# Kernel optimization log

Measured on AMD Instinct MI355X. Metric: run time of the kernel, lower is better.

## Reference

```python
import math
import jax, jax.numpy as jnp
import numpy as np

B, N, TOKEN_DIM = 8, 8192, 512
NODE_DIM = 64
MAX_NODES = 64
SCORE_HIDDEN = 64


def setup_inputs() -> dict:
    key = jax.random.key(0)
    ks = jax.random.split(key, 8)
    s = lambda k, shape, fan_in: jax.random.normal(k, shape, jnp.float32) / np.sqrt(fan_in)
    return {
        "token_feats": jax.random.normal(ks[0], (B, N, TOKEN_DIM), jnp.float32),
        "score_w1": s(ks[1], (TOKEN_DIM, SCORE_HIDDEN), TOKEN_DIM),
        "score_b1": jnp.zeros((SCORE_HIDDEN,), jnp.float32),
        "score_w2": s(ks[2], (SCORE_HIDDEN, 1), SCORE_HIDDEN),
        "score_b2": jnp.zeros((1,), jnp.float32),
        "t2n_w": s(ks[3], (TOKEN_DIM, NODE_DIM), TOKEN_DIM),
        "n2t_w": s(ks[4], (NODE_DIM, TOKEN_DIM), NODE_DIM),
        "gcn_w1": s(ks[5], (NODE_DIM, NODE_DIM), NODE_DIM),
        "gcn_w2": s(ks[6], (NODE_DIM, NODE_DIM), NODE_DIM),
    }


def reference(token_feats, score_w1, score_b1, score_w2, score_b2,
              t2n_w, n2t_w, gcn_w1, gcn_w2):
    Bn, Nn, d = token_feats.shape
    M = MAX_NODES
    eps = 1e-6

    # --- node selection (scores -> threshold -> top-k among selected) ---
    h = jax.nn.relu(jnp.einsum('bnd,dh->bnh', token_feats, score_w1) + score_b1)
    scores = (jnp.einsum('bnh,ho->bno', h, score_w2) + score_b2)[..., 0]  # [B,N]
    mean = scores.mean(axis=1, keepdims=True)
    std = scores.std(axis=1, keepdims=True)  # unbiased=False (population)
    thr = mean + 0.5 * std
    count = jnp.sum(scores > thr, axis=1)  # [B]
    fallback_k = min(M, max(4, Nn // 16))
    take_k = jnp.where(count == 0, fallback_k, jnp.minimum(count, M))  # [B]

    _, top_idx = jax.lax.top_k(scores, M)  # [B,M] highest scores; set == torch's selection
    node_mask = jnp.arange(M)[None, :] < take_k[:, None]  # [B,M] bool
    maskf = node_mask.astype(token_feats.dtype)

    gathered = jnp.take_along_axis(token_feats, top_idx[..., None], axis=1)  # [B,M,d]
    H0 = jnp.einsum('bmd,dk->bmk', gathered, t2n_w) * maskf[..., None]  # [B,M,node_dim]

    # --- cosine-similarity adjacency, masked, self-loops, row-normalized ---
    nrm = jnp.maximum(jnp.linalg.norm(H0, axis=-1, keepdims=True), eps)
    Hn = H0 / nrm
    A = jax.nn.relu(jnp.einsum('bik,bjk->bij', Hn, Hn))
    A = A * (maskf[:, :, None] * maskf[:, None, :])
    A = A + jnp.eye(M, dtype=A.dtype)[None] * maskf[:, None, :]
    A = A / jnp.maximum(A.sum(axis=-1, keepdims=True), 1e-6)

    # --- two-layer GCN (no bias) ---
    x = jax.nn.relu(jnp.einsum('bij,bjk,kl->bil', A, H0, gcn_w1))
    Hg = jax.nn.relu(jnp.einsum('bij,bjk,kl->bil', A, x, gcn_w2))  # [B,M,node_dim]

    # --- attention scatter-back to tokens ---
    token_proj = jnp.einsum('bnd,dk->bnk', token_feats, t2n_w)  # [B,N,node_dim]
    logits = jnp.einsum('bnk,bmk->bnm', token_proj, Hg) / math.sqrt(NODE_DIM)
    attn = jax.nn.softmax(logits, axis=-1)
    injected = jnp.einsum('bnm,bmk->bnk', attn, Hg)
    back = jnp.einsum('bnk,kd->bnd', injected, n2t_w)
    return token_feats + back
```

## Files before the change

kernel.cpp:

```cpp
#include <hip/hip_runtime.h>
#include <hip/hip_bf16.h>

#define B_ 8
#define N_ 8192
#define D_ 512
#define M_ 64

typedef unsigned short u16;
typedef unsigned int u32;
typedef __attribute__((ext_vector_type(8))) short bf16x8;
typedef __attribute__((ext_vector_type(4))) float f32x4;

__device__ __forceinline__ u16 f2bf(float f) {
  u32 u = __float_as_uint(f);
  u += 0x7FFFu + ((u >> 16) & 1u);
  return (u16)(u >> 16);
}
__device__ __forceinline__ float bf2f(u16 h) {
  return __uint_as_float(((u32)h) << 16);
}

__device__ __forceinline__ int bfrag_idx(int kd, int c, int ncols16) {
  int sub = (kd >> 5) * ncols16 + (c >> 4);
  int lane = (c & 15) + 16 * ((kd & 15) >> 2);
  int e = (kd & 3) + 4 * ((kd >> 4) & 1);
  return sub * 512 + lane * 8 + e;
}

__device__ __forceinline__ int kslot(int ln, int e) {
  return (e & 3) + 4 * (ln >> 4) + 16 * (e >> 2);
}

__device__ __forceinline__ bf16x8 pack8(float4 v0, float4 v1) {
  bf16x8 a;
  a[0] = (short)f2bf(v0.x); a[1] = (short)f2bf(v0.y);
  a[2] = (short)f2bf(v0.z); a[3] = (short)f2bf(v0.w);
  a[4] = (short)f2bf(v1.x); a[5] = (short)f2bf(v1.y);
  a[6] = (short)f2bf(v1.z); a[7] = (short)f2bf(v1.w);
  return a;
}

__global__ __launch_bounds__(256) void k_prep(
    const float* __restrict__ t2n, const float* __restrict__ n2t,
    const float* __restrict__ W1, const float* __restrict__ g1,
    const float* __restrict__ g2,
    u16* __restrict__ t2nf, u16* __restrict__ n2tf,
    u16* __restrict__ W1h, u16* __restrict__ W1l,
    u16* __restrict__ g1f, u16* __restrict__ g2f)
{
  const int gid = blockIdx.x * 256 + threadIdx.x;
  const int stride = gridDim.x * 256;
  for (int s = gid; s < 512 * 64; s += stride) {
    const int k = s >> 6, c = s & 63;
    const int idx = bfrag_idx(k, c, 4);
    t2nf[idx] = f2bf(t2n[s]);
    const float w = W1[s];
    const u16 wh = f2bf(w);
    W1h[idx] = wh;
    W1l[idx] = f2bf(w - bf2f(wh));
  }
  for (int s = gid; s < 64 * 512; s += stride) {
    const int k = s >> 9, c = s & 511;
    n2tf[bfrag_idx(k, c, 32)] = f2bf(n2t[s]);
  }
  for (int s = gid; s < 4096; s += stride) {
    const int k = s >> 6, c = s & 63;
    g1f[bfrag_idx(k, c, 4)] = f2bf(g1[s]);
    g2f[bfrag_idx(k, c, 4)] = f2bf(g2[s]);
  }
}

__global__ __launch_bounds__(256, 3) void k_sp(
    const float* __restrict__ X, const u16* __restrict__ W1h,
    const u16* __restrict__ W1l, const u16* __restrict__ t2nf,
    const float* __restrict__ b1, const float* __restrict__ w2,
    const float* __restrict__ b2, float* __restrict__ scores,
    float* __restrict__ outStash)
{
  __shared__ __align__(16) u16 sAf[4096];
  const int tid = threadIdx.x;
  const int t0 = blockIdx.x * 64;
  const int wv = tid >> 6, ln = tid & 63;
  const int lq = ln >> 4, lr = ln & 15;
  u16* mySf = &sAf[wv * 1024];
  const float* xr = X + (size_t)(t0 + 16 * wv + lr) * D_;

  f32x4 acc[4], accP[4];
  #pragma unroll
  for (int cb = 0; cb < 4; ++cb) {
    acc[cb] = (f32x4){0.f, 0.f, 0.f, 0.f};
    accP[cb] = (f32x4){0.f, 0.f, 0.f, 0.f};
  }

  float4 p0[3], p1[3];
  #pragma unroll
  for (int q = 0; q < 3; ++q) {
    p0[q] = *(const float4*)(xr + 32 * q + 4 * lq);
    p1[q] = *(const float4*)(xr + 32 * q + 16 + 4 * lq);
  }

  #pragma unroll
  for (int kb = 0; kb < 16; ++kb) {
    const int slot = kb % 3;
    const float4 v0 = p0[slot], v1 = p1[slot];
    if (kb + 3 < 16) {
      p0[slot] = *(const float4*)(xr + 32 * (kb + 3) + 4 * lq);
      p1[slot] = *(const float4*)(xr + 32 * (kb + 3) + 16 + 4 * lq);
    }
    const float xs[8] = {v0.x, v0.y, v0.z, v0.w, v1.x, v1.y, v1.z, v1.w};
    bf16x8 ah, al;
    #pragma unroll
    for (int e = 0; e < 8; ++e) {
      const u16 h = f2bf(xs[e]);
      ah[e] = (short)h;
      al[e] = (short)f2bf(xs[e] - bf2f(h));
    }
    #pragma unroll
    for (int cb = 0; cb < 4; ++cb) {
      const bf16x8 bh = *(const bf16x8*)&W1h[(kb * 4 + cb) * 512 + ln * 8];
      const bf16x8 bl = *(const bf16x8*)&W1l[(kb * 4 + cb) * 512 + ln * 8];
      const bf16x8 bt = *(const bf16x8*)&t2nf[(kb * 4 + cb) * 512 + ln * 8];
      acc[cb]  = __builtin_amdgcn_mfma_f32_16x16x32_bf16(ah, bh, acc[cb], 0, 0, 0);
      acc[cb]  = __builtin_amdgcn_mfma_f32_16x16x32_bf16(ah, bl, acc[cb], 0, 0, 0);
      acc[cb]  = __builtin_amdgcn_mfma_f32_16x16x32_bf16(al, bh, acc[cb], 0, 0, 0);
      accP[cb] = __builtin_amdgcn_mfma_f32_16x16x32_bf16(ah, bt, accP[cb], 0, 0, 0);
    }
  }

  float b1v[4], w2v[4];
  #pragma unroll
  for (int cb = 0; cb < 4; ++cb) {
    const int col = cb * 16 + lr;
    b1v[cb] = b1[col]; w2v[cb] = w2[col];
  }
  const float b2v = b2[0];
  #pragma unroll
  for (int r = 0; r < 4; ++r) {
    float p = 0.f;
    #pragma unroll
    for (int cb = 0; cb < 4; ++cb) {
      const float h = fmaxf(acc[cb][r] + b1v[cb], 0.f);
      p = fmaf(h, w2v[cb], p);
    }
    p += __shfl_xor(p, 1); p += __shfl_xor(p, 2);
    p += __shfl_xor(p, 4); p += __shfl_xor(p, 8);
    if (lr == 0) scores[t0 + wv * 16 + 4 * lq + r] = p + b2v;
  }

  #pragma unroll
  for (int cb = 0; cb < 4; ++cb)
    #pragma unroll
    for (int r = 0; r < 4; ++r) {
      const int idx = (cb >> 1) * 512 + (4 * lq + r + 16 * (lr >> 2)) * 8 +
                      (lr & 3) + 4 * (cb & 1);
      mySf[idx] = f2bf(accP[cb][r]);
    }
  u16* stash = (u16*)(outStash + (size_t)blockIdx.x * 32768);
  #pragma unroll
  for (int kb2 = 0; kb2 < 2; ++kb2)
    *(bf16x8*)&stash[wv * 1024 + kb2 * 512 + ln * 8] =
        *(const bf16x8*)&mySf[kb2 * 512 + ln * 8];
}

__global__ __launch_bounds__(1024) void k_select(
    const float* __restrict__ scores, int* __restrict__ top_idx,
    int* __restrict__ take_k)
{
  __shared__ float sS[N_];
  __shared__ u32 hist[256];
  __shared__ float redf[34];
  __shared__ u32 redu[16];
  __shared__ u32 sPrefix, sRank, sCntA, sCntT;
  __shared__ int candIdx[64];
  __shared__ float candVal[64];
  __shared__ int tieIdx[128];
  const int b = blockIdx.x, tid = threadIdx.x;
  const int wv = tid >> 6, ln = tid & 63;
  const float* s = scores + (size_t)b * N_;

  float sum = 0.f, sq = 0.f;
  for (int i = tid; i < N_; i += 1024) {
    const float v = s[i]; sS[i] = v; sum += v; sq = fmaf(v, v, sq);
  }
  #pragma unroll
  for (int off = 32; off > 0; off >>= 1) {
    sum += __shfl_xor(sum, off);
    sq  += __shfl_xor(sq, off);
  }
  if (ln == 0) { redf[wv] = sum; redf[16 + wv] = sq; }
  __syncthreads();
  if (tid == 0) {
    float tot = 0.f, totq = 0.f;
    #pragma unroll
    for (int w = 0; w < 16; ++w) { tot += redf[w]; totq += redf[16 + w]; }
    const float mean = tot / (float)N_;
    const float var  = totq / (float)N_ - mean * mean;
    redf[32] = mean + 0.5f * sqrtf(fmaxf(var, 0.f));
  }
  __syncthreads();
  const float thr = redf[32];
  int c = 0;
  for (int i = tid; i < N_; i += 1024) c += (sS[i] > thr) ? 1 : 0;
  #pragma unroll
  for (int off = 32; off > 0; off >>= 1) c += __shfl_xor(c, off);
  if (ln == 0) redu[wv] = (u32)c;
  __syncthreads();
  if (tid == 0) {
    int cnt = 0;
    #pragma unroll
    for (int w = 0; w < 16; ++w) cnt += (int)redu[w];
    take_k[b] = (cnt == 0) ? M_ : (cnt < M_ ? cnt : M_);
  }
  __syncthreads();

  u32 prefix = 0, rank = 64, pmask = 0;
  for (int pass = 0; pass < 4; ++pass) {
    const int shift = 24 - 8 * pass;
    if (tid < 256) hist[tid] = 0;
    __syncthreads();
    for (int i = tid; i < N_; i += 1024) {
      const u32 u = __float_as_uint(sS[i]);
      const u32 key = u ^ ((u32)((int)u >> 31) | 0x80000000u);
      const bool active = (key & pmask) == prefix;
      const int bin = (int)((key >> shift) & 255u);
      if (pass == 0) {
        unsigned long long act = __ballot(active);
        while (act) {
          const int leader = (int)__builtin_ctzll(act);
          const int lbin = __shfl(bin, leader);
          const unsigned long long eq = __ballot(active && (bin == lbin));
          if (ln == leader) atomicAdd(&hist[lbin], (u32)__builtin_popcountll(eq));
          act &= ~eq;
        }
      } else {
        if (active) atomicAdd(&hist[bin], 1u);
      }
    }
    __syncthreads();
    if (tid < 64) {
      const u32 h0 = hist[4 * tid], h1 = hist[4 * tid + 1];
      const u32 h2 = hist[4 * tid + 2], h3 = hist[4 * tid + 3];
      const u32 s3 = h3, s2 = h2 + s3, s1 = h1 + s2, s0 = h0 + s1;
      u32 run = s0;
      #pragma unroll
      for (int off = 1; off < 64; off <<= 1) {
        const u32 t = (u32)__shfl_down((int)run, off);
        if (tid + off < 64) run += t;
      }
      const u32 excl = run - s0;
      const u32 c0 = s0 + excl, c1 = s1 + excl, c2 = s2 + excl, c3 = s3 + excl;
      int pick = -1; u32 nxt = 0;
      if (c0 >= rank && c1 < rank)        { pick = 0; nxt = c1; }
      else if (c1 >= rank && c2 < rank)   { pick = 1; nxt = c2; }
      else if (c2 >= rank && c3 < rank)   { pick = 2; nxt = c3; }
      else if (c3 >= rank && excl < rank) { pick = 3; nxt = excl; }
      if (pick >= 0) {
        sPrefix = prefix | ((u32)(4 * tid + pick) << shift);
        sRank = rank - nxt;
      }
    }
    __syncthreads();
    prefix = sPrefix; rank = sRank;
    pmask |= 0xFFu << shift;
    __syncthreads();
  }

  if (tid == 0) { sCntA = 0; sCntT = 0; }
  __syncthreads();
  const u32 pivot = prefix;
  for (int i = tid; i < N_; i += 1024) {
    const u32 u = __float_as_uint(sS[i]);
    const u32 key = u ^ ((u32)((int)u >> 31) | 0x80000000u);
    if (key > pivot) {
      const u32 p = atomicAdd(&sCntA, 1u);
      candIdx[p] = i; candVal[p] = sS[i];
    } else if (key == pivot) {
      const u32 p = atomicAdd(&sCntT, 1u);
      if (p < 128) tieIdx[p] = i;
    }
  }
  __syncthreads();
  if (tid == 0) {
    const int nA = (int)sCntA;
    const int need = 64 - nA;
    int nT = (int)sCntT; if (nT > 128) nT = 128;
    for (int j = 0; j < need; ++j) {
      int bi = 1 << 30, bp = -1;
      for (int q = 0; q < nT; ++q) {
        const int v = tieIdx[q];
        if (v >= 0 && v < bi) { bi = v; bp = q; }
      }
      candIdx[nA + j] = bi; candVal[nA + j] = sS[bi]; tieIdx[bp] = -1;
    }
  }
  __syncthreads();
  if (tid < 64) {
    const float v = candVal[tid]; const int ii = candIdx[tid];
    int rk = 0;
    for (int j = 0; j < 64; ++j) {
      const float vj = candVal[j]; const int ij = candIdx[j];
      rk += (vj > v || (vj == v && ij < ii)) ? 1 : 0;
    }
    top_idx[b * M_ + rk] = ii;
  }
}

__device__ __forceinline__ bf16x8 ldsA_frag(const float (*S)[65], int wv, int kb, int ln) {
  const int lr = ln & 15;
  bf16x8 a;
  #pragma unroll
  for (int e = 0; e < 8; ++e) a[e] = (short)f2bf(S[16 * wv + lr][32 * kb + kslot(ln, e)]);
  return a;
}
__device__ __forceinline__ bf16x8 ldsB_frag(const float (*S)[65], int cb, int kb, int ln) {
  const int lr = ln & 15;
  bf16x8 bb;
  #pragma unroll
  for (int e = 0; e < 8; ++e) bb[e] = (short)f2bf(S[32 * kb + kslot(ln, e)][16 * cb + lr]);
  return bb;
}
__device__ __forceinline__ bf16x8 ldsBT_frag(const float (*S)[65], int cb, int kb, int ln) {
  const int lr = ln & 15;
  bf16x8 bb;
  #pragma unroll
  for (int e = 0; e < 8; ++e) bb[e] = (short)f2bf(S[16 * cb + lr][32 * kb + kslot(ln, e)]);
  return bb;
}

__global__ __launch_bounds__(256) void k_graph(
    const float* __restrict__ X, const u16* __restrict__ t2nf,
    const u16* __restrict__ n2tf, const u16* __restrict__ g1f,
    const u16* __restrict__ g2f, const int* __restrict__ top_idx,
    const int* __restrict__ take_k, u16* __restrict__ HgTf,
    u16* __restrict__ Wf)
{
  __shared__ float sH0[64][65];
  __shared__ float sA[64][65];
  __shared__ float sT[64][65];
  __shared__ float sU[64][65];
  __shared__ float sR[64];
  const int b = blockIdx.x, tid = threadIdx.x;
  const int wv = tid >> 6, ln = tid & 63;
  const int lq = ln >> 4, lr = ln & 15;
  const int tk = take_k[b];
  const int rowm = 16 * wv + 4 * lq;

  const int gidx = top_idx[b * M_ + 16 * wv + lr];
  const float* xr = X + ((size_t)b * N_ + gidx) * D_;
  f32x4 d[4];
  #pragma unroll
  for (int cb = 0; cb < 4; ++cb) d[cb] = (f32x4){0.f, 0.f, 0.f, 0.f};
  {
    float4 p0[3], p1[3];
    #pragma unroll
    for (int q = 0; q < 3; ++q) {
      p0[q] = *(const float4*)(xr + 32 * q + 4 * lq);
      p1[q] = *(const float4*)(xr + 32 * q + 16 + 4 * lq);
    }
    #pragma unroll
    for (int kb = 0; kb < 16; ++kb) {
      const int slot = kb % 3;
      const float4 v0 = p0[slot], v1 = p1[slot];
      if (kb + 3 < 16) {
        p0[slot] = *(const float4*)(xr + 32 * (kb + 3) + 4 * lq);
        p1[slot] = *(const float4*)(xr + 32 * (kb + 3) + 16 + 4 * lq);
      }
      const bf16x8 a = pack8(v0, v1);
      #pragma unroll
      for (int cb = 0; cb < 4; ++cb) {
        const bf16x8 bb = *(const bf16x8*)&t2nf[(kb * 4 + cb) * 512 + ln * 8];
        d[cb] = __builtin_amdgcn_mfma_f32_16x16x32_bf16(a, bb, d[cb], 0, 0, 0);
      }
    }
  }
  #pragma unroll
  for (int cb = 0; cb < 4; ++cb)
    #pragma unroll
    for (int r = 0; r < 4; ++r)
      sH0[rowm + r][16 * cb + lr] = (rowm + r < tk) ? d[cb][r] : 0.f;
  __syncthreads();

  if (tid < 64) {
    float s = 0.f;
    #pragma unroll
    for (int k = 0; k < 64; ++k) { const float v = sH0[tid][k]; s = fmaf(v, v, s); }
    sR[tid] = 1.f / fmaxf(sqrtf(s), 1e-6f);
  }
  __syncthreads();
  #pragma unroll
  for (int p = 0; p < 16; ++p) {
    const int o = tid + p * 256;
    const int i = o >> 6, k = o & 63;
    sU[i][k] = sH0[i][k] * sR[i];
  }
  __syncthreads();

  #pragma unroll
  for (int cb = 0; cb < 4; ++cb) d[cb] = (f32x4){0.f, 0.f, 0.f, 0.f};
  #pragma unroll
  for (int kb = 0; kb < 2; ++kb) {
    const bf16x8 a = ldsA_frag(sU, wv, kb, ln);
    #pragma unroll
    for (int cb = 0; cb < 4; ++cb)
      d[cb] = __builtin_amdgcn_mfma_f32_16x16x32_bf16(a, ldsBT_frag(sU, cb, kb, ln), d[cb], 0, 0, 0);
  }
  __syncthreads();
  #pragma unroll
  for (int cb = 0; cb < 4; ++cb)
    #pragma unroll
    for (int r = 0; r < 4; ++r) {
      const int row = rowm + r, col = 16 * cb + lr;
      float s = fmaxf(d[cb][r], 0.f);
      s = (row < tk && col < tk) ? s : 0.f;
      if (row == col && row < tk) s += 1.f;
      sA[row][col] = s;
    }
  __syncthreads();

  if (tid < 64) {
    float rs = 0.f;
    #pragma unroll
    for (int j = 0; j < 64; ++j) rs += sA[tid][j];
    sR[tid] = 1.f / fmaxf(rs, 1e-6f);
  }
  __syncthreads();
  #pragma unroll
  for (int p = 0; p < 16; ++p) {
    const int o = tid + p * 256;
    const int i = o >> 6, j = o & 63;
    sA[i][j] *= sR[i];
  }
  __syncthreads();

  #pragma unroll
  for (int cb = 0; cb < 4; ++cb) d[cb] = (f32x4){0.f, 0.f, 0.f, 0.f};
  #pragma unroll
  for (int kb = 0; kb < 2; ++kb) {
    const bf16x8 a = ldsA_frag(sA, wv, kb, ln);
    #pragma unroll
    for (int cb = 0; cb < 4; ++cb)
      d[cb] = __builtin_amdgcn_mfma_f32_16x16x32_bf16(a, ldsB_frag(sH0, cb, kb, ln), d[cb], 0, 0, 0);
  }
  __syncthreads();
  #pragma unroll
  for (int cb = 0; cb < 4; ++cb)
    #pragma unroll
    for (int r = 0; r < 4; ++r) sT[rowm + r][16 * cb + lr] = d[cb][r];
  __syncthreads();

  #pragma unroll
  for (int cb = 0; cb < 4; ++cb) d[cb] = (f32x4){0.f, 0.f, 0.f, 0.f};
  #pragma unroll
  for (int kb = 0; kb < 2; ++kb) {
    const bf16x8 a = ldsA_frag(sT, wv, kb, ln);
    #pragma unroll
    for (int cb = 0; cb < 4; ++cb) {
      const bf16x8 bb = *(const bf16x8*)&g1f[(kb * 4 + cb) * 512 + ln * 8];
      d[cb] = __builtin_amdgcn_mfma_f32_16x16x32_bf16(a, bb, d[cb], 0, 0, 0);
    }
  }
  __syncthreads();
  #pragma unroll
  for (int cb = 0; cb < 4; ++cb)
    #pragma unroll
    for (int r = 0; r < 4; ++r) sU[rowm + r][16 * cb + lr] = fmaxf(d[cb][r], 0.f);
  __syncthreads();

  #pragma unroll
  for (int cb = 0; cb < 4; ++cb) d[cb] = (f32x4){0.f, 0.f, 0.f, 0.f};
  #pragma unroll
  for (int kb = 0; kb < 2; ++kb) {
    const bf16x8 a = ldsA_frag(sA, wv, kb, ln);
    #pragma unroll
    for (int cb = 0; cb < 4; ++cb)
      d[cb] = __builtin_amdgcn_mfma_f32_16x16x32_bf16(a, ldsB_frag(sU, cb, kb, ln), d[cb], 0, 0, 0);
  }
  __syncthreads();
  #pragma unroll
  for (int cb = 0; cb < 4; ++cb)
    #pragma unroll
    for (int r = 0; r < 4; ++r) sT[rowm + r][16 * cb + lr] = d[cb][r];
  __syncthreads();

  #pragma unroll
  for (int cb = 0; cb < 4; ++cb) d[cb] = (f32x4){0.f, 0.f, 0.f, 0.f};
  #pragma unroll
  for (int kb = 0; kb < 2; ++kb) {
    const bf16x8 a = ldsA_frag(sT, wv, kb, ln);
    #pragma unroll
    for (int cb = 0; cb < 4; ++cb) {
      const bf16x8 bb = *(const bf16x8*)&g2f[(kb * 4 + cb) * 512 + ln * 8];
      d[cb] = __builtin_amdgcn_mfma_f32_16x16x32_bf16(a, bb, d[cb], 0, 0, 0);
    }
  }
  __syncthreads();
  #pragma unroll
  for (int cb = 0; cb < 4; ++cb)
    #pragma unroll
    for (int r = 0; r < 4; ++r) {
      const int node = rowm + r, feat = 16 * cb + lr;
      const float hv = fmaxf(d[cb][r], 0.f);
      HgTf[(size_t)b * 4096 + bfrag_idx(feat, node, 4)] = f2bf(hv);
      sU[node][feat] = hv;
    }
  __syncthreads();

  for (int chk = 0; chk < 4; ++chk) {
    f32x4 aw[8];
    #pragma unroll
    for (int c8 = 0; c8 < 8; ++c8) aw[c8] = (f32x4){0.f, 0.f, 0.f, 0.f};
    #pragma unroll
    for (int kbf = 0; kbf < 2; ++kbf) {
      const bf16x8 a = ldsA_frag(sU, wv, kbf, ln);
      #pragma unroll
      for (int c8 = 0; c8 < 8; ++c8) {
        const bf16x8 bb = *(const bf16x8*)&n2tf[(kbf * 32 + chk * 8 + c8) * 512 + ln * 8];
        aw[c8] = __builtin_amdgcn_mfma_f32_16x16x32_bf16(a, bb, aw[c8], 0, 0, 0);
      }
    }
    #pragma unroll
    for (int c8 = 0; c8 < 8; ++c8)
      #pragma unroll
      for (int r = 0; r < 4; ++r) {
        const int m = 16 * wv + 4 * lq + r;
        const int c = (chk * 8 + c8) * 16 + lr;
        Wf[(size_t)b * 32768 + bfrag_idx(m, c, 32)] = f2bf(aw[c8][r]);
      }
  }
}

__global__ __launch_bounds__(256) void k_attn(
    const float* __restrict__ X, const u16* __restrict__ HgTf,
    const u16* __restrict__ Wf, float* __restrict__ out)
{
  __shared__ __align__(16) u16 sAf[4096];
  __shared__ __align__(16) float sBo[4][16][68];
  const int tid = threadIdx.x;
  const int b = blockIdx.x >> 7;
  const int t0 = (blockIdx.x & 127) << 6;
  const float* Xb = X + (size_t)b * N_ * D_;
  float* Ob = out + (size_t)b * N_ * D_;
  const int wv = tid >> 6, ln = tid & 63;
  const int lq = ln >> 4, lr = ln & 15;
  u16* mySf = &sAf[wv * 1024];
  const u16* stash = (const u16*)(out + (size_t)blockIdx.x * 32768);

  f32x4 accL[4];
  #pragma unroll
  for (int cb = 0; cb < 4; ++cb) accL[cb] = (f32x4){0.f, 0.f, 0.f, 0.f};
  #pragma unroll
  for (int kb = 0; kb < 2; ++kb) {
    const bf16x8 a = *(const bf16x8*)&stash[wv * 1024 + kb * 512 + ln * 8];
    #pragma unroll
    for (int cb = 0; cb < 4; ++cb) {
      const bf16x8 bb = *(const bf16x8*)&HgTf[(size_t)b * 4096 + (kb * 4 + cb) * 512 + ln * 8];
      accL[cb] = __builtin_amdgcn_mfma_f32_16x16x32_bf16(a, bb, accL[cb], 0, 0, 0);
    }
  }
  __syncthreads();

  float attnv[4][4];
  #pragma unroll
  for (int r = 0; r < 4; ++r) {
    const float v0 = accL[0][r], v1 = accL[1][r], v2 = accL[2][r], v3 = accL[3][r];
    float mx = fmaxf(fmaxf(v0, v1), fmaxf(v2, v3));
    mx = fmaxf(mx, __shfl_xor(mx, 1)); mx = fmaxf(mx, __shfl_xor(mx, 2));
    mx = fmaxf(mx, __shfl_xor(mx, 4)); mx = fmaxf(mx, __shfl_xor(mx, 8));
    const float e0 = __expf((v0 - mx) * 0.125f), e1 = __expf((v1 - mx) * 0.125f);
    const float e2 = __expf((v2 - mx) * 0.125f), e3 = __expf((v3 - mx) * 0.125f);
    float sm = (e0 + e1) + (e2 + e3);
    sm += __shfl_xor(sm, 1); sm += __shfl_xor(sm, 2);
    sm += __shfl_xor(sm, 4); sm += __shfl_xor(sm, 8);
    const float inv = 1.f / sm;
    attnv[0][r] = e0 * inv; attnv[1][r] = e1 * inv;
    attnv[2][r] = e2 * inv; attnv[3][r] = e3 * inv;
  }
  #pragma unroll
  for (int cb = 0; cb < 4; ++cb)
    #pragma unroll
    for (int r = 0; r < 4; ++r) {
      const int idx = (cb >> 1) * 512 + (4 * lq + r + 16 * (lr >> 2)) * 8 +
                      (lr & 3) + 4 * (cb & 1);
      mySf[idx] = f2bf(attnv[cb][r]);
    }

  for (int chk = 0; chk < 4; ++chk) {
    float4 xres[8];
    #pragma unroll
    for (int h = 0; h < 2; ++h)
      #pragma unroll
      for (int j = 0; j < 4; ++j)
        xres[h * 4 + j] = *(const float4*)(
            Xb + (size_t)(t0 + 16 * wv + 4 * j + lq) * D_ + chk * 128 + h * 64 + 4 * lr);

    f32x4 accB[8];
    #pragma unroll
    for (int c8 = 0; c8 < 8; ++c8) accB[c8] = (f32x4){0.f, 0.f, 0.f, 0.f};
    #pragma unroll
    for (int kb = 0; kb < 2; ++kb) {
      const bf16x8 a = *(const bf16x8*)&mySf[kb * 512 + ln * 8];
      #pragma unroll
      for (int c8 = 0; c8 < 8; ++c8) {
        const bf16x8 bb = *(const bf16x8*)&Wf[(size_t)b * 32768 + (kb * 32 + chk * 8 + c8) * 512 + ln * 8];
        accB[c8] = __builtin_amdgcn_mfma_f32_16x16x32_bf16(a, bb, accB[c8], 0, 0, 0);
      }
    }
    #pragma unroll
    for (int h = 0; h < 2; ++h) {
      #pragma unroll
      for (int c4 = 0; c4 < 4; ++c4)
        #pragma unroll
        for (int r = 0; r < 4; ++r)
          sBo[wv][4 * lq + r][c4 * 16 + lr] = accB[4 * h + c4][r];
      #pragma unroll
      for (int j = 0; j < 4; ++j) {
        const int rloc = 4 * j + lq;
        float4 v = *(const float4*)&sBo[wv][rloc][4 * lr];
        const float4 xv = xres[h * 4 + j];
        v.x += xv.x; v.y += xv.y; v.z += xv.z; v.w += xv.w;
        *(float4*)(Ob + (size_t)(t0 + 16 * wv + rloc) * D_ + chk * 128 + h * 64 + 4 * lr) = v;
      }
    }
  }
}

extern "C" void kernel_launch(void* const* d_in, const int* in_sizes, int n_in,
                              void* d_out, int out_size, void* d_ws, size_t ws_size,
                              hipStream_t stream)
{
  (void)in_sizes; (void)n_in; (void)out_size; (void)ws_size;
  const float* X   = (const float*)d_in[0];
  const float* W1  = (const float*)d_in[1];
  const float* b1  = (const float*)d_in[2];
  const float* w2  = (const float*)d_in[3];
  const float* b2  = (const float*)d_in[4];
  const float* t2n = (const float*)d_in[5];
  const float* n2t = (const float*)d_in[6];
  const float* g1  = (const float*)d_in[7];
  const float* g2  = (const float*)d_in[8];
  float* out = (float*)d_out;

  char* ws = (char*)d_ws;
  float* scores = (float*)(ws);
  u16* t2nf     = (u16*)(ws + 262144);
  u16* n2tf     = (u16*)(ws + 327680);
  u16* W1h      = (u16*)(ws + 393216);
  u16* W1l      = (u16*)(ws + 458752);
  u16* HgTf     = (u16*)(ws + 524288);
  u16* g1f      = (u16*)(ws + 589824);
  u16* g2f      = (u16*)(ws + 598016);
  int* top_idx  = (int*)(ws + 606208);
  int* take_k   = (int*)(ws + 608256);
  u16* Wf       = (u16*)(ws + 609280);

  k_prep<<<64, 256, 0, stream>>>(t2n, n2t, W1, g1, g2, t2nf, n2tf, W1h, W1l, g1f, g2f);
  k_sp<<<1024, 256, 0, stream>>>(X, W1h, W1l, t2nf, b1, w2, b2, scores, out);
  k_select<<<B_, 1024, 0, stream>>>(scores, top_idx, take_k);
  k_graph<<<B_, 256, 0, stream>>>(X, t2nf, n2tf, g1f, g2f, top_idx, take_k, HgTf, Wf);
  k_attn<<<1024, 256, 0, stream>>>(X, HgTf, Wf, out);
}
```

Measured before the change: 145.9 us.

## Stage weight fragments in shared memory cooperatively instead of per-wave global loads

Each of the four waves used to load all three weight fragment sets (W1 hi, W1 lo, t2n) from global memory for every k-block. Now each wave loads a quarter of them into registers, writes them to a shared buffer, and all waves read from LDS after a barrier, with the next k-block prefetched. The token prefetch depth drops from three stages to one, and the occupancy hint goes from 3 to 4 blocks. This cuts redundant global/L2 traffic but adds two block barriers per k-step and a shallower X prefetch, which could expose latency.

```diff
diff --git a/kernel.cpp b/kernel.cpp
--- a/kernel.cpp
+++ b/kernel.cpp
@@ -70,13 +70,14 @@
   }
 }
 
-__global__ __launch_bounds__(256, 3) void k_sp(
+__global__ __launch_bounds__(256, 4) void k_sp(
     const float* __restrict__ X, const u16* __restrict__ W1h,
     const u16* __restrict__ W1l, const u16* __restrict__ t2nf,
     const float* __restrict__ b1, const float* __restrict__ w2,
     const float* __restrict__ b2, float* __restrict__ scores,
     float* __restrict__ outStash)
 {
+  __shared__ __align__(16) u16 sB[6144];
   __shared__ __align__(16) u16 sAf[4096];
   const int tid = threadIdx.x;
   const int t0 = blockIdx.x * 64;
@@ -92,20 +93,30 @@
     accP[cb] = (f32x4){0.f, 0.f, 0.f, 0.f};
   }
 
-  float4 p0[3], p1[3];
-  #pragma unroll
-  for (int q = 0; q < 3; ++q) {
-    p0[q] = *(const float4*)(xr + 32 * q + 4 * lq);
-    p1[q] = *(const float4*)(xr + 32 * q + 16 + 4 * lq);
-  }
-
-  #pragma unroll
+  auto gsrc = [&](int f, int kb) -> const u16* {
+    const int cb = f / 3, mat = f % 3;
+    const u16* mp = (mat == 0) ? W1h : (mat == 1) ? W1l : t2nf;
+    return mp + (kb * 4 + cb) * 512 + ln * 8;
+  };
+
+  bf16x8 wr[3];
+  #pragma unroll
+  for (int j = 0; j < 3; ++j) wr[j] = *(const bf16x8*)gsrc(j * 4 + wv, 0);
+  float4 va0 = *(const float4*)(xr + 4 * lq);
+  float4 va1 = *(const float4*)(xr + 16 + 4 * lq);
+
   for (int kb = 0; kb < 16; ++kb) {
-    const int slot = kb % 3;
-    const float4 v0 = p0[slot], v1 = p1[slot];
-    if (kb + 3 < 16) {
-      p0[slot] = *(const float4*)(xr + 32 * (kb + 3) + 4 * lq);
-      p1[slot] = *(const float4*)(xr + 32 * (kb + 3) + 16 + 4 * lq);
+    __syncthreads();
+    #pragma unroll
+    for (int j = 0; j < 3; ++j)
+      *(bf16x8*)&sB[(j * 4 + wv) * 512 + ln * 8] = wr[j];
+    __syncthreads();
+    const float4 v0 = va0, v1 = va1;
+    if (kb < 15) {
+      #pragma unroll
+      for (int j = 0; j < 3; ++j) wr[j] = *(const bf16x8*)gsrc(j * 4 + wv, kb + 1);
+      va0 = *(const float4*)(xr + 32 * (kb + 1) + 4 * lq);
+      va1 = *(const float4*)(xr + 32 * (kb + 1) + 16 + 4 * lq);
     }
     const float xs[8] = {v0.x, v0.y, v0.z, v0.w, v1.x, v1.y, v1.z, v1.w};
     bf16x8 ah, al;
@@ -117,9 +128,9 @@
     }
     #pragma unroll
     for (int cb = 0; cb < 4; ++cb) {
-      const bf16x8 bh = *(const bf16x8*)&W1h[(kb * 4 + cb) * 512 + ln * 8];
-      const bf16x8 bl = *(const bf16x8*)&W1l[(kb * 4 + cb) * 512 + ln * 8];
-      const bf16x8 bt = *(const bf16x8*)&t2nf[(kb * 4 + cb) * 512 + ln * 8];
+      const bf16x8 bh = *(const bf16x8*)&sB[(cb * 3 + 0) * 512 + ln * 8];
+      const bf16x8 bl = *(const bf16x8*)&sB[(cb * 3 + 1) * 512 + ln * 8];
+      const bf16x8 bt = *(const bf16x8*)&sB[(cb * 3 + 2) * 512 + ln * 8];
       acc[cb]  = __builtin_amdgcn_mfma_f32_16x16x32_bf16(ah, bh, acc[cb], 0, 0, 0);
       acc[cb]  = __builtin_amdgcn_mfma_f32_16x16x32_bf16(ah, bl, acc[cb], 0, 0, 0);
       acc[cb]  = __builtin_amdgcn_mfma_f32_16x16x32_bf16(al, bh, acc[cb], 0, 0, 0);
```

Result: faster. 132.3 us (-9.4%).
